# Kernel tuning notes

Hardware: AMD Instinct MI355X
Metric: run time of the kernel (lower is better)

Reference implementation:

```python
import math
import jax, jax.numpy as jnp
import numpy as np

B, T, C = 2, 2048, 2048
NQ, NKV, H = 16, 4, 128
EPS = 1e-6
ROPE_BASE = 5.0e6


def setup_inputs() -> dict:
    key = jax.random.key(0)
    ks = jax.random.split(key, 6)
    x = jax.random.normal(ks[0], (B, T, C), dtype=jnp.float32)
    s = 0.02
    Wq = jax.random.normal(ks[1], (C, NQ * H), dtype=jnp.float32) * s
    Wk = jax.random.normal(ks[2], (C, NKV * H), dtype=jnp.float32) * s
    Wv = jax.random.normal(ks[3], (C, NKV * H), dtype=jnp.float32) * s
    Wo = jax.random.normal(ks[4], (NQ * H, C), dtype=jnp.float32) * s
    q_norm_w = jnp.ones((H,), dtype=jnp.float32)
    k_norm_w = jnp.ones((H,), dtype=jnp.float32)
    # RoPE tables (seq_start = 0)
    inv_freq = 1.0 / (ROPE_BASE ** (jnp.arange(0, H, 2, dtype=jnp.float32) / H))
    t = jnp.arange(T, dtype=jnp.float32)
    freqs = jnp.einsum('i,j->ij', t, inv_freq)          # [T, H/2]
    emb = jnp.concatenate([freqs, freqs], axis=-1)       # [T, H]
    cos = jnp.cos(emb)
    sin = jnp.sin(emb)
    # additive causal mask (finite large negative to stay nan-free)
    causal = jnp.tril(jnp.ones((T, T), dtype=bool))
    attn_mask = jnp.where(causal, 0.0, -1e9).astype(jnp.float32)
    return {"x": x, "Wq": Wq, "Wk": Wk, "Wv": Wv, "Wo": Wo,
            "q_norm_w": q_norm_w, "k_norm_w": k_norm_w,
            "cos": cos, "sin": sin, "attn_mask": attn_mask}


def _rms_norm(x, w):
    # x: [..., H]
    var = jnp.mean(x * x, axis=-1, keepdims=True)
    return w * (x * jax.lax.rsqrt(var + EPS))


def _rotate_half(x):
    x1, x2 = jnp.split(x, 2, axis=-1)
    return jnp.concatenate([-x2, x1], axis=-1)


def reference(x, Wq, Wk, Wv, Wo, q_norm_w, k_norm_w, cos, sin, attn_mask):
    q = (x @ Wq).reshape(B, T, NQ, H)
    k = (x @ Wk).reshape(B, T, NKV, H)
    v = (x @ Wv).reshape(B, T, NKV, H)
    q = _rms_norm(q, q_norm_w)
    k = _rms_norm(k, k_norm_w)
    c = cos[None, :, None, :]  # [1,T,1,H]
    s = sin[None, :, None, :]
    q = q * c + _rotate_half(q) * s
    k = k * c + _rotate_half(k) * s
    rep = NQ // NKV
    k = jnp.repeat(k, rep, axis=2)  # [B,T,NQ,H]
    v = jnp.repeat(v, rep, axis=2)
    scores = jnp.einsum('bihd,bjhd->bhij', q, k) / math.sqrt(H)
    scores = scores + attn_mask[None, None, :, :]
    probs = jax.nn.softmax(scores, axis=-1)
    ctx = jnp.einsum('bhij,bjhd->bihd', probs, v).reshape(B, T, NQ * H)
    return ctx @ Wo
```

## Files before the change

kernel.cpp:

```cpp
#include <hip/hip_runtime.h>
#include <hip/hip_bf16.h>

#define B_   2
#define T_   2048
#define C_   2048
#define NQ_  16
#define NKV_ 4
#define H_   128

using bf16x8 = __attribute__((ext_vector_type(8))) short;
using f32x4  = __attribute__((ext_vector_type(4))) float;

__device__ __forceinline__ unsigned short f2bf(float f) {
    __hip_bfloat16 h = __float2bfloat16(f);
    union { __hip_bfloat16 h; unsigned short s; } c;
    c.h = h;
    return c.s;
}
__device__ __forceinline__ float bf2f(unsigned short s) {
    return __uint_as_float(((unsigned)s) << 16);
}
__device__ __forceinline__ bf16x8 pack8(float4 f0, float4 f1) {
    bf16x8 r;
    r[0] = (short)f2bf(f0.x); r[1] = (short)f2bf(f0.y);
    r[2] = (short)f2bf(f0.z); r[3] = (short)f2bf(f0.w);
    r[4] = (short)f2bf(f1.x); r[5] = (short)f2bf(f1.y);
    r[6] = (short)f2bf(f1.z); r[7] = (short)f2bf(f1.w);
    return r;
}

#define MFMA16(a, b, c) __builtin_amdgcn_mfma_f32_16x16x32_bf16(a, b, c, 0, 0, 0)

__device__ __forceinline__ void gl_lds16(const void* g, void* l) {
    __builtin_amdgcn_global_load_lds(
        (const __attribute__((address_space(1))) void*)g,
        (__attribute__((address_space(3))) void*)l, 16, 0, 0);
}

__global__ void transpose_cvt(const float* __restrict__ src,
                              unsigned short* __restrict__ dst,
                              int R, int Cc) {
    const int tc = Cc >> 6;
    const int r0 = (blockIdx.x / tc) * 64;
    const int c0 = (blockIdx.x % tc) * 64;
    __shared__ unsigned short Tl[64 * 65];
    const int tid = threadIdx.x;
#pragma unroll
    for (int it = 0; it < 16; ++it) {
        const int idx = it * 256 + tid;
        const int r = idx >> 6, c = idx & 63;
        Tl[c * 65 + r] = f2bf(src[(size_t)(r0 + r) * Cc + c0 + c]);
    }
    __syncthreads();
#pragma unroll
    for (int it = 0; it < 16; ++it) {
        const int idx = it * 256 + tid;
        const int c = idx >> 6, r = idx & 63;
        dst[(size_t)(c0 + c) * R + r0 + r] = Tl[c * 65 + r];
    }
}

#define LDP 40

template <bool A_BF, bool OUT_F32>
__global__ __launch_bounds__(256, 2) void gemm_bt(
    const void* __restrict__ Av,
    const unsigned short* __restrict__ Bt,
    void* __restrict__ Cqv,
    unsigned short* __restrict__ Ck,
    unsigned short* __restrict__ Cv,
    int M, int N, int K, int fused) {
    const int ntn = N >> 7;
    const int tm  = blockIdx.x / ntn;
    const int tn  = blockIdx.x % ntn;

    const int tid  = threadIdx.x;
    const int wv   = tid >> 6;
    const int lane = tid & 63;
    const int col  = lane & 15;
    const int quad = lane >> 4;
    const int wm   = (wv & 1) * 64;
    const int wn   = (wv >> 1) * 64;

    __shared__ unsigned short Al[128 * LDP];
    __shared__ unsigned short Bl[128 * LDP];

    f32x4 acc[4][4];
#pragma unroll
    for (int mt = 0; mt < 4; ++mt)
#pragma unroll
        for (int nt = 0; nt < 4; ++nt) acc[mt][nt] = (f32x4){0.f, 0.f, 0.f, 0.f};

    const int i1 = tid, i2 = tid + 256;
    const size_t aoff1 = (size_t)(tm * 128 + (i1 >> 2)) * K + (i1 & 3) * 8;
    const size_t aoff2 = (size_t)(tm * 128 + (i2 >> 2)) * K + (i2 & 3) * 8;
    const size_t boff1 = (size_t)(tn * 128 + (i1 >> 2)) * K + (i1 & 3) * 8;
    const size_t boff2 = (size_t)(tn * 128 + (i2 >> 2)) * K + (i2 & 3) * 8;
    unsigned short* Aw1 = Al + (i1 >> 2) * LDP + (i1 & 3) * 8;
    unsigned short* Aw2 = Al + (i2 >> 2) * LDP + (i2 & 3) * 8;
    unsigned short* Bw1 = Bl + (i1 >> 2) * LDP + (i1 & 3) * 8;
    unsigned short* Bw2 = Bl + (i2 >> 2) * LDP + (i2 & 3) * 8;

    const unsigned short* Ab16 = (const unsigned short*)Av;
    const float*          Af   = (const float*)Av;

    uint4  a1u, a2u, b1u, b2u;
    float4 a1lo, a1hi, a2lo, a2hi;

    auto loadAB = [&](int kk) {
        if constexpr (A_BF) {
            a1u = *(const uint4*)(Ab16 + aoff1 + kk);
            a2u = *(const uint4*)(Ab16 + aoff2 + kk);
        } else {
            a1lo = *(const float4*)(Af + aoff1 + kk);
            a1hi = *(const float4*)(Af + aoff1 + kk + 4);
            a2lo = *(const float4*)(Af + aoff2 + kk);
            a2hi = *(const float4*)(Af + aoff2 + kk + 4);
        }
        b1u = *(const uint4*)(Bt + boff1 + kk);
        b2u = *(const uint4*)(Bt + boff2 + kk);
    };

    loadAB(0);

    for (int k0 = 0; k0 < K; k0 += 32) {
        __syncthreads();
        if constexpr (A_BF) {
            *(uint4*)Aw1 = a1u;
            *(uint4*)Aw2 = a2u;
        } else {
            *(bf16x8*)Aw1 = pack8(a1lo, a1hi);
            *(bf16x8*)Aw2 = pack8(a2lo, a2hi);
        }
        *(uint4*)Bw1 = b1u;
        *(uint4*)Bw2 = b2u;
        __syncthreads();

        const int kn = (k0 + 32 < K) ? k0 + 32 : k0;
        loadAB(kn);

        bf16x8 af[4], bfv[4];
#pragma unroll
        for (int t = 0; t < 4; ++t) {
            af[t]  = *(const bf16x8*)(Al + (wm + t * 16 + col) * LDP + quad * 8);
            bfv[t] = *(const bf16x8*)(Bl + (wn + t * 16 + col) * LDP + quad * 8);
        }
#pragma unroll
        for (int mt = 0; mt < 4; ++mt)
#pragma unroll
            for (int nt = 0; nt < 4; ++nt)
                acc[mt][nt] = MFMA16(af[mt], bfv[nt], acc[mt][nt]);
    }

    const int nb = tn * 128;
    if constexpr (OUT_F32) {
        float* Co = (float*)Cqv;
#pragma unroll
        for (int mt = 0; mt < 4; ++mt)
#pragma unroll
            for (int nt = 0; nt < 4; ++nt)
#pragma unroll
                for (int r = 0; r < 4; ++r) {
                    const int row = tm * 128 + wm + mt * 16 + quad * 4 + r;
                    const int cc  = nb + wn + nt * 16 + col;
                    Co[(size_t)row * N + cc] = acc[mt][nt][r];
                }
    } else {
        unsigned short* Cb;
        int ldc, nc0;
        if (!fused)         { Cb = (unsigned short*)Cqv; ldc = N;    nc0 = nb;        }
        else if (nb < 2048) { Cb = (unsigned short*)Cqv; ldc = 2048; nc0 = nb;        }
        else if (nb < 2560) { Cb = Ck;                   ldc = 512;  nc0 = nb - 2048; }
        else                { Cb = Cv;                   ldc = 512;  nc0 = nb - 2560; }
#pragma unroll
        for (int mt = 0; mt < 4; ++mt)
#pragma unroll
            for (int nt = 0; nt < 4; ++nt)
#pragma unroll
                for (int r = 0; r < 4; ++r) {
                    const int row = tm * 128 + wm + mt * 16 + quad * 4 + r;
                    const int cc  = nc0 + wn + nt * 16 + col;
                    Cb[(size_t)row * ldc + cc] = f2bf(acc[mt][nt][r]);
                }
    }
}

__global__ void norm_rope(unsigned short* __restrict__ buf,
                          const float* __restrict__ w,
                          const float* __restrict__ cosb,
                          const float* __restrict__ sinb,
                          int nheads, float oscale) {
    const int idx = blockIdx.x;
    const int h   = idx % nheads;
    const int bt  = idx / nheads;
    const int t   = bt % T_;
    unsigned short* row = buf + ((size_t)bt * nheads + h) * H_;
    const int l = threadIdx.x;

    const float x0 = bf2f(row[l]);
    const float x1 = bf2f(row[l + 64]);
    float ss = x0 * x0 + x1 * x1;
#pragma unroll
    for (int off = 32; off; off >>= 1) ss += __shfl_xor(ss, off);
    const float r = rsqrtf(ss * (1.0f / 128.0f) + 1e-6f) * oscale;

    const float n0 = x0 * r * w[l];
    const float n1 = x1 * r * w[l + 64];
    const float c0 = cosb[t * H_ + l];
    const float c1 = cosb[t * H_ + l + 64];
    const float s0 = sinb[t * H_ + l];
    const float s1 = sinb[t * H_ + l + 64];

    row[l]      = f2bf(n0 * c0 - n1 * s0);
    row[l + 64] = f2bf(n1 * c1 + n0 * s1);
}

__global__ __launch_bounds__(256, 3) void flash_attn(
    const unsigned short* __restrict__ qbuf,
    const unsigned short* __restrict__ kbuf,
    const unsigned short* __restrict__ vbuf,
    unsigned short* __restrict__ ctx) {
    const int blk = blockIdx.x;
    const int lo  = blk & 15;
    const int bh  = blk >> 4;
    const int qt  = (bh & 16) ? (15 - lo) : lo;
    const int h   = bh & 15;
    const int b   = bh >> 4;
    const int kvh = h >> 2;

    const int tid  = threadIdx.x;
    const int wave = tid >> 6;
    const int lane = tid & 63;
    const int col  = lane & 15;
    const int quad = lane >> 4;

    const int qbase = qt * 128;
    const int w0    = qbase + wave * 32;

    __shared__ unsigned short Kl[64 * 128];
    __shared__ unsigned short Vt[128 * 72];
    __shared__ unsigned short Pl[4][32 * 72];
    __shared__ float alf[4][32];

    bf16x8 qf[2][4];
#pragma unroll
    for (int nt = 0; nt < 2; ++nt)
#pragma unroll
        for (int ks = 0; ks < 4; ++ks) {
            const size_t off =
                ((size_t)(b * T_ + w0 + nt * 16 + col) * NQ_ + h) * H_ + ks * 32 + quad * 8;
            qf[nt][ks] = *(const bf16x8*)(qbuf + off);
        }

    f32x4 O[2][8];
#pragma unroll
    for (int pt = 0; pt < 2; ++pt)
#pragma unroll
        for (int dt = 0; dt < 8; ++dt) O[pt][dt] = (f32x4){0.f, 0.f, 0.f, 0.f};
    float m_run[2] = {-3.0e38f, -3.0e38f};
    float l_run[2] = {0.f, 0.f};

    const int swb = (col & 7) << 4;
    unsigned short* Pw = Pl[wave];
    unsigned* Vw = (unsigned*)Vt;
    const int nch = 2 * qt + 2;

    for (int c = 0; c < nch; ++c) {
        const int j0 = c * 64;
        __syncthreads();

#pragma unroll
        for (int i = 0; i < 4; ++i) {
            const int row = wave * 16 + i * 4 + quad;
            const unsigned short* g =
                kbuf + ((size_t)(b * T_ + j0 + row) * NKV_ + kvh) * H_ +
                ((col ^ ((i * 4 + quad) & 7)) << 3);
            gl_lds16(g, Kl + wave * 2048 + i * 512);
        }
#pragma unroll
        for (int it = 0; it < 2; ++it) {
            const int idx = it * 256 + tid;
            const int kp  = idx & 31;
            const int dc  = idx >> 5;
            const size_t g0 = ((size_t)(b * T_ + j0 + 2 * kp) * NKV_ + kvh) * H_ + dc * 8;
            const uint4 v0 = *(const uint4*)(vbuf + g0);
            const uint4 v1 = *(const uint4*)(vbuf + g0 + (size_t)NKV_ * H_);
            const int wb = dc * 8 * 36 + kp;
            Vw[wb + 0 * 36] = (v0.x & 0xFFFFu) | (v1.x << 16);
            Vw[wb + 1 * 36] = (v0.x >> 16)     | (v1.x & 0xFFFF0000u);
            Vw[wb + 2 * 36] = (v0.y & 0xFFFFu) | (v1.y << 16);
            Vw[wb + 3 * 36] = (v0.y >> 16)     | (v1.y & 0xFFFF0000u);
            Vw[wb + 4 * 36] = (v0.z & 0xFFFFu) | (v1.z << 16);
            Vw[wb + 5 * 36] = (v0.z >> 16)     | (v1.z & 0xFFFF0000u);
            Vw[wb + 6 * 36] = (v0.w & 0xFFFFu) | (v1.w << 16);
            Vw[wb + 7 * 36] = (v0.w >> 16)     | (v1.w & 0xFFFF0000u);
        }
        __syncthreads();

        if (j0 > w0 + 31) continue;

        f32x4 St[4][2];
#pragma unroll
        for (int mt = 0; mt < 4; ++mt)
#pragma unroll
            for (int nt = 0; nt < 2; ++nt) St[mt][nt] = (f32x4){0.f, 0.f, 0.f, 0.f};
#pragma unroll
        for (int ks = 0; ks < 4; ++ks)
#pragma unroll
            for (int mt = 0; mt < 4; ++mt) {
                const bf16x8 kfrag = *(const bf16x8*)(
                    Kl + ((mt * 16 + col) << 7) + (((ks * 64 + quad * 16) ^ swb) >> 1));
                St[mt][0] = MFMA16(kfrag, qf[0][ks], St[mt][0]);
                St[mt][1] = MFMA16(kfrag, qf[1][ks], St[mt][1]);
            }

        const bool needmask = (j0 + 63 > w0);
        if (needmask) {
            const int ig0 = w0 + col;
#pragma unroll
            for (int mt = 0; mt < 4; ++mt)
#pragma unroll
                for (int r = 0; r < 4; ++r) {
                    const int key = j0 + mt * 16 + quad * 4 + r;
                    if (key > ig0)      St[mt][0][r] = -3.0e38f;
                    if (key > ig0 + 16) St[mt][1][r] = -3.0e38f;
                }
        }

        float rm[2];
#pragma unroll
        for (int nt = 0; nt < 2; ++nt) {
            float m0 = fmaxf(fmaxf(St[0][nt][0], St[0][nt][1]),
                             fmaxf(St[0][nt][2], St[0][nt][3]));
#pragma unroll
            for (int mt = 1; mt < 4; ++mt)
                m0 = fmaxf(m0, fmaxf(fmaxf(St[mt][nt][0], St[mt][nt][1]),
                                     fmaxf(St[mt][nt][2], St[mt][nt][3])));
            m0 = fmaxf(m0, __shfl_xor(m0, 16));
            m0 = fmaxf(m0, __shfl_xor(m0, 32));
            rm[nt] = m0;
        }

        const int defer = __all((rm[0] <= m_run[0] + 8.0f) && (rm[1] <= m_run[1] + 8.0f));
        if (!defer) {
            const float mn0 = fmaxf(m_run[0], rm[0]);
            const float mn1 = fmaxf(m_run[1], rm[1]);
            const float al0 = exp2f(m_run[0] - mn0);
            const float al1 = exp2f(m_run[1] - mn1);
            m_run[0] = mn0; m_run[1] = mn1;
            l_run[0] *= al0; l_run[1] *= al1;
            if (quad == 0) { alf[wave][col] = al0; alf[wave][col + 16] = al1; }
        }

        float ls0 = 0.f, ls1 = 0.f;
#pragma unroll
        for (int mt = 0; mt < 4; ++mt) {
            const float p0 = exp2f(St[mt][0][0] - m_run[0]);
            const float p1 = exp2f(St[mt][0][1] - m_run[0]);
            const float p2 = exp2f(St[mt][0][2] - m_run[0]);
            const float p3 = exp2f(St[mt][0][3] - m_run[0]);
            ls0 += (p0 + p1) + (p2 + p3);
            *(uint2*)(Pw + col * 72 + mt * 16 + quad * 4) =
                make_uint2((unsigned)f2bf(p0) | ((unsigned)f2bf(p1) << 16),
                           (unsigned)f2bf(p2) | ((unsigned)f2bf(p3) << 16));
            const float q0 = exp2f(St[mt][1][0] - m_run[1]);
            const float q1 = exp2f(St[mt][1][1] - m_run[1]);
            const float q2 = exp2f(St[mt][1][2] - m_run[1]);
            const float q3 = exp2f(St[mt][1][3] - m_run[1]);
            ls1 += (q0 + q1) + (q2 + q3);
            *(uint2*)(Pw + (col + 16) * 72 + mt * 16 + quad * 4) =
                make_uint2((unsigned)f2bf(q0) | ((unsigned)f2bf(q1) << 16),
                           (unsigned)f2bf(q2) | ((unsigned)f2bf(q3) << 16));
        }
        ls0 += __shfl_xor(ls0, 16); ls0 += __shfl_xor(ls0, 32);
        ls1 += __shfl_xor(ls1, 16); ls1 += __shfl_xor(ls1, 32);
        l_run[0] += ls0; l_run[1] += ls1;

        if (!defer) {
            const f32x4 a0 = *(const f32x4*)&alf[wave][quad * 4];
            const f32x4 a1 = *(const f32x4*)&alf[wave][quad * 4 + 16];
#pragma unroll
            for (int dt = 0; dt < 8; ++dt)
#pragma unroll
                for (int r = 0; r < 4; ++r) { O[0][dt][r] *= a0[r]; O[1][dt][r] *= a1[r]; }
        }

#pragma unroll
        for (int ks = 0; ks < 2; ++ks) {
            const bf16x8 pa0 = *(const bf16x8*)(Pw + col * 72 + ks * 32 + quad * 8);
            const bf16x8 pa1 = *(const bf16x8*)(Pw + (col + 16) * 72 + ks * 32 + quad * 8);
#pragma unroll
            for (int dt = 0; dt < 8; ++dt) {
                const bf16x8 vf = *(const bf16x8*)(Vt + (dt * 16 + col) * 72 + ks * 32 + quad * 8);
                O[0][dt] = MFMA16(pa0, vf, O[0][dt]);
                O[1][dt] = MFMA16(pa1, vf, O[1][dt]);
            }
        }
    }

    if (quad == 0) {
        alf[wave][col]      = 1.0f / l_run[0];
        alf[wave][col + 16] = 1.0f / l_run[1];
    }
    const f32x4 i0 = *(const f32x4*)&alf[wave][quad * 4];
    const f32x4 i1 = *(const f32x4*)&alf[wave][quad * 4 + 16];
#pragma unroll
    for (int pt = 0; pt < 2; ++pt)
#pragma unroll
        for (int r = 0; r < 4; ++r) {
            const float inv = pt ? i1[r] : i0[r];
            const int ig = w0 + pt * 16 + quad * 4 + r;
            unsigned short* op = ctx + ((size_t)(b * T_ + ig) * NQ_ + h) * H_;
#pragma unroll
            for (int dt = 0; dt < 8; ++dt)
                op[dt * 16 + col] = f2bf(O[pt][dt][r] * inv);
        }
}

extern "C" void kernel_launch(void* const* d_in, const int* in_sizes, int n_in,
                              void* d_out, int out_size, void* d_ws, size_t ws_size,
                              hipStream_t stream) {
    const float* x    = (const float*)d_in[0];
    const float* Wq   = (const float*)d_in[1];
    const float* Wk   = (const float*)d_in[2];
    const float* Wv   = (const float*)d_in[3];
    const float* Wo   = (const float*)d_in[4];
    const float* qnw  = (const float*)d_in[5];
    const float* knw  = (const float*)d_in[6];
    const float* cosb = (const float*)d_in[7];
    const float* sinb = (const float*)d_in[8];

    const int M = B_ * T_;
    unsigned short* ws  = (unsigned short*)d_ws;
    unsigned short* WqT = ws;
    unsigned short* WkT = WqT + (size_t)2048 * 2048;
    unsigned short* WvT = WkT + (size_t)512 * 2048;
    unsigned short* ctx = ws;
    unsigned short* q   = ws + (size_t)8388608;
    unsigned short* k   = ws + (size_t)16777216;
    unsigned short* v   = ws + (size_t)18874368;
    unsigned short* WoT = q;

    transpose_cvt<<<(2048 / 64) * (2048 / 64), 256, 0, stream>>>(Wq, WqT, 2048, 2048);
    transpose_cvt<<<(2048 / 64) * (512 / 64),  256, 0, stream>>>(Wk, WkT, 2048, 512);
    transpose_cvt<<<(2048 / 64) * (512 / 64),  256, 0, stream>>>(Wv, WvT, 2048, 512);

    gemm_bt<false, false><<<(M / 128) * (3072 / 128), 256, 0, stream>>>(
        (const void*)x, WqT, (void*)q, k, v, M, 3072, C_, 1);

    norm_rope<<<M * NQ_, 64, 0, stream>>>(q, qnw, cosb, sinb, NQ_, 0.12751743f);
    norm_rope<<<M * NKV_, 64, 0, stream>>>(k, knw, cosb, sinb, NKV_, 1.0f);

    flash_attn<<<512, 256, 0, stream>>>(q, k, v, ctx);

    transpose_cvt<<<(2048 / 64) * (2048 / 64), 256, 0, stream>>>(Wo, WoT, 2048, 2048);
    gemm_bt<true, true><<<(M / 128) * (C_ / 128), 256, 0, stream>>>(
        (const void*)ctx, WoT, d_out, nullptr, nullptr, M, C_, NQ_ * H_, 0);
}
```

Baseline: 414.8 us.

## Prefetch next K/V tile into registers to overlap loads with compute

Replaces the direct global-to-LDS K loads and synchronous V loads with a register-staged software pipeline. The next chunk's K and V are issued into registers before the current chunk's attention math, then written to LDS after the next barrier. This hides global memory latency behind compute. In exchange it uses more registers, so the launch bounds occupancy hint drops from 3 to 2 blocks per CU.

```diff
diff --git a/kernel.cpp b/kernel.cpp
--- a/kernel.cpp
+++ b/kernel.cpp
@@ -30,12 +30,6 @@
 }
 
 #define MFMA16(a, b, c) __builtin_amdgcn_mfma_f32_16x16x32_bf16(a, b, c, 0, 0, 0)
-
-__device__ __forceinline__ void gl_lds16(const void* g, void* l) {
-    __builtin_amdgcn_global_load_lds(
-        (const __attribute__((address_space(1))) void*)g,
-        (__attribute__((address_space(3))) void*)l, 16, 0, 0);
-}
 
 __global__ void transpose_cvt(const float* __restrict__ src,
                               unsigned short* __restrict__ dst,
@@ -215,7 +209,7 @@
     row[l + 64] = f2bf(n1 * c1 + n0 * s1);
 }
 
-__global__ __launch_bounds__(256, 3) void flash_attn(
+__global__ __launch_bounds__(256, 2) void flash_attn(
     const unsigned short* __restrict__ qbuf,
     const unsigned short* __restrict__ kbuf,
     const unsigned short* __restrict__ vbuf,
@@ -265,27 +259,45 @@
     unsigned* Vw = (unsigned*)Vt;
     const int nch = 2 * qt + 2;
 
-    for (int c = 0; c < nch; ++c) {
-        const int j0 = c * 64;
-        __syncthreads();
-
+    uint4 ka[4], va[4];
+    const size_t kvstride = (size_t)NKV_ * H_;
+
+    auto issueK = [&](int j0) {
 #pragma unroll
         for (int i = 0; i < 4; ++i) {
             const int row = wave * 16 + i * 4 + quad;
-            const unsigned short* g =
+            ka[i] = *(const uint4*)(
                 kbuf + ((size_t)(b * T_ + j0 + row) * NKV_ + kvh) * H_ +
-                ((col ^ ((i * 4 + quad) & 7)) << 3);
-            gl_lds16(g, Kl + wave * 2048 + i * 512);
-        }
+                ((col ^ (row & 7)) << 3));
+        }
+    };
+    auto issueV = [&](int j0) {
 #pragma unroll
         for (int it = 0; it < 2; ++it) {
             const int idx = it * 256 + tid;
             const int kp  = idx & 31;
             const int dc  = idx >> 5;
             const size_t g0 = ((size_t)(b * T_ + j0 + 2 * kp) * NKV_ + kvh) * H_ + dc * 8;
-            const uint4 v0 = *(const uint4*)(vbuf + g0);
-            const uint4 v1 = *(const uint4*)(vbuf + g0 + (size_t)NKV_ * H_);
-            const int wb = dc * 8 * 36 + kp;
+            va[2 * it]     = *(const uint4*)(vbuf + g0);
+            va[2 * it + 1] = *(const uint4*)(vbuf + g0 + kvstride);
+        }
+    };
+    auto writeK = [&]() {
+#pragma unroll
+        for (int i = 0; i < 4; ++i) {
+            const int row = wave * 16 + i * 4 + quad;
+            *(uint4*)(Kl + row * 128 + col * 8) = ka[i];
+        }
+    };
+    auto writeV = [&]() {
+#pragma unroll
+        for (int it = 0; it < 2; ++it) {
+            const int idx = it * 256 + tid;
+            const int kp  = idx & 31;
+            const int dc  = idx >> 5;
+            const uint4 v0 = va[2 * it];
+            const uint4 v1 = va[2 * it + 1];
+            const int wb = dc * 288 + kp;
             Vw[wb + 0 * 36] = (v0.x & 0xFFFFu) | (v1.x << 16);
             Vw[wb + 1 * 36] = (v0.x >> 16)     | (v1.x & 0xFFFF0000u);
             Vw[wb + 2 * 36] = (v0.y & 0xFFFFu) | (v1.y << 16);
@@ -295,7 +307,22 @@
             Vw[wb + 6 * 36] = (v0.w & 0xFFFFu) | (v1.w << 16);
             Vw[wb + 7 * 36] = (v0.w >> 16)     | (v1.w & 0xFFFF0000u);
         }
+    };
+
+    issueK(0);
+    issueV(0);
+
+    for (int c = 0; c < nch; ++c) {
+        const int j0 = c * 64;
         __syncthreads();
+        writeK();
+        writeV();
+        __syncthreads();
+
+        if (c + 1 < nch) {
+            issueK(j0 + 64);
+            issueV(j0 + 64);
+        }
 
         if (j0 > w0 + 31) continue;
 
```

Measured after the change: 420.0 us. No clear change (+1.3%).
